# Kernel tuning notes

Hardware: AMD Instinct MI355X
Metric: run time of the kernel (lower is better)

## Reference

```python
import jax, jax.numpy as jnp
import numpy as np
import math

D = 512
H = 8
DH = D // H
B, T = 4, 2048


def _poly(x, coeffs):
    # iterative-power polynomial eval, same products as the Vandermonde matmul
    acc = coeffs[0] * jnp.ones_like(x)
    p = jnp.ones_like(x)
    for i in range(1, coeffs.shape[0]):
        p = p * x
        acc = acc + coeffs[i] * p
    return acc


def _exp_fn(x, exp_c):
    return jnp.maximum(_poly(x, exp_c), 1e-8)


def _softmax(x, exp_c):
    x = x - jnp.max(x, axis=-1, keepdims=True)
    e = _exp_fn(x, exp_c)
    return e / jnp.sum(e, axis=-1, keepdims=True)


def _gelu(x, gelu_c):
    return _poly(jnp.clip(x, -4.0, 4.0), gelu_c)


def _layernorm(x, gamma, beta):
    mean = jnp.mean(x, axis=-1, keepdims=True)
    var = jnp.mean(x * x, axis=-1, keepdims=True) - mean * mean
    v = var + 1e-5
    y = jnp.full_like(v, 0.5)
    for _ in range(3):  # Newton iterations for rsqrt
        y = y * (3.0 - v * y * y) * 0.5
    return (x - mean) * y * gamma + beta


def setup_inputs() -> dict:
    key = jax.random.key(0)
    ks = jax.random.split(key, 8)
    x = jax.random.normal(ks[0], (B, T, D), dtype=jnp.float32)
    s = 0.02
    Wq = jax.random.normal(ks[1], (D, D), dtype=jnp.float32) * s
    Wk = jax.random.normal(ks[2], (D, D), dtype=jnp.float32) * s
    Wv = jax.random.normal(ks[3], (D, D), dtype=jnp.float32) * s
    Wo = jax.random.normal(ks[4], (D, D), dtype=jnp.float32) * s
    W1 = jax.random.normal(ks[5], (D, 4 * D), dtype=jnp.float32) * s
    W2 = jax.random.normal(ks[6], (4 * D, D), dtype=jnp.float32) * s
    g1 = jnp.ones((D,), jnp.float32); b1 = jnp.zeros((D,), jnp.float32)
    g2 = jnp.ones((D,), jnp.float32); b2 = jnp.zeros((D,), jnp.float32)
    # GELU degree-7 least-squares fit on [-4,4]
    x_fit = jnp.linspace(-4.0, 4.0, 1000)
    y_fit = 0.5 * x_fit * (1.0 + jax.scipy.special.erf(x_fit / math.sqrt(2.0)))
    V = x_fit[:, None] ** jnp.arange(8)[None, :]
    gelu_c = jnp.linalg.lstsq(V, y_fit)[0].astype(jnp.float32)
    # exp Taylor coeffs degree 6
    exp_c = jnp.array([1.0 / math.factorial(i) for i in range(7)], dtype=jnp.float32)
    return dict(x=x, Wq=Wq, Wk=Wk, Wv=Wv, Wo=Wo, W1=W1, W2=W2,
                g1=g1, b1=b1, g2=g2, b2=b2, gelu_c=gelu_c, exp_c=exp_c)


def reference(x, Wq, Wk, Wv, Wo, W1, W2, g1, b1, g2, b2, gelu_c, exp_c):
    Bn, Tn, Dn = x.shape
    q = (x @ Wq).reshape(Bn, Tn, H, DH).transpose(0, 2, 1, 3)  # [B,H,T,dh]
    k = (x @ Wk).reshape(Bn, Tn, H, DH).transpose(0, 2, 1, 3)
    v = (x @ Wv).reshape(Bn, Tn, H, DH).transpose(0, 2, 1, 3)
    scores = jnp.einsum('bhqd,bhkd->bhqk', q, k) / math.sqrt(DH)
    attn = _softmax(scores, exp_c)
    out = jnp.einsum('bhqk,bhkd->bhqd', attn, v).transpose(0, 2, 1, 3).reshape(Bn, Tn, Dn)
    out = out @ Wo
    h = _layernorm(x + out, g1, b1)
    ffn = _gelu(h @ W1, gelu_c) @ W2
    return _layernorm(h + ffn, g2, b2)
```

## Files before the change

### kernel.cpp

```cpp
#include <hip/hip_runtime.h>
#include <hip/hip_bf16.h>

typedef __bf16 bf16_t;
typedef __bf16 bf16x8 __attribute__((ext_vector_type(8)));
typedef float f32x4 __attribute__((ext_vector_type(4)));

#define MFMA16(a, b, c) __builtin_amdgcn_mfma_f32_16x16x32_bf16((a), (b), (c), 0, 0, 0)

__device__ __forceinline__ void gl_lds16(const bf16_t* g, bf16_t* l) {
  __builtin_amdgcn_global_load_lds(
      (const __attribute__((address_space(1))) void*)g,
      (__attribute__((address_space(3))) void*)l, 16, 0, 0);
}

__device__ __forceinline__ unsigned pack_bf16(float a, float b) {
  union { bf16_t h[2]; unsigned u; } c;
  c.h[0] = (bf16_t)a; c.h[1] = (bf16_t)b;
  return c.u;
}

__global__ __launch_bounds__(256) void k_prep(
    const float* __restrict__ x, bf16_t* __restrict__ x_bf,
    const float* __restrict__ Wq, const float* __restrict__ Wk,
    const float* __restrict__ Wv, const float* __restrict__ Wo,
    const float* __restrict__ W1, const float* __restrict__ W2,
    bf16_t* __restrict__ WqkvT, bf16_t* __restrict__ WoT,
    bf16_t* __restrict__ W1T, bf16_t* __restrict__ W2T) {
  __shared__ float tile[64][65];
  int bid = blockIdx.x, tid = threadIdx.x;
  if (bid < 4096) {
    int i = bid * 256 + tid;
    float4 f = ((const float4*)x)[i];
    union { bf16_t h[4]; uint2 u; } cv;
    cv.h[0] = (bf16_t)f.x; cv.h[1] = (bf16_t)f.y;
    cv.h[2] = (bf16_t)f.z; cv.h[3] = (bf16_t)f.w;
    ((uint2*)x_bf)[i] = cv.u;
    return;
  }
  int t = bid - 4096;
  const float* W; bf16_t* WT; int K, N, idx, gx;
  if (t < 64)       { W = Wq; WT = WqkvT;                      K = 512;  N = 512;  idx = t;       gx = 8;  }
  else if (t < 128) { W = Wk; WT = WqkvT + (size_t)512 * 512;  K = 512;  N = 512;  idx = t - 64;  gx = 8;  }
  else if (t < 192) { W = Wv; WT = WqkvT + (size_t)1024 * 512; K = 512;  N = 512;  idx = t - 128; gx = 8;  }
  else if (t < 256) { W = Wo; WT = WoT;                        K = 512;  N = 512;  idx = t - 192; gx = 8;  }
  else if (t < 512) { W = W1; WT = W1T;                        K = 512;  N = 2048; idx = t - 256; gx = 8;  }
  else              { W = W2; WT = W2T;                        K = 2048; N = 512;  idx = t - 512; gx = 32; }
  int bk = (idx % gx) * 64, bn = (idx / gx) * 64;
  int tx = tid & 63, ty = tid >> 6;
  for (int i = ty; i < 64; i += 4)
    tile[i][tx] = W[(size_t)(bk + i) * N + bn + tx];
  __syncthreads();
  for (int i = ty; i < 64; i += 4)
    WT[(size_t)(bn + i) * K + bk + tx] = (bf16_t)tile[tx][i];
}

template <int MODE, int BM>
__global__ __launch_bounds__(256) void k_gemm_bt(
    const bf16_t* __restrict__ A, const bf16_t* __restrict__ Bt,
    float* __restrict__ Cf, bf16_t* __restrict__ Cb,
    bf16_t* __restrict__ Cb2, bf16_t* __restrict__ Cb3,
    int M, int N, int K, const float* __restrict__ coef) {
  __shared__ __align__(16) bf16_t As[2][BM * 32];
  __shared__ __align__(16) bf16_t Bs[2][128 * 32];
  constexpr int NF = (BM == 128) ? 4 : 2;
  int tid = threadIdx.x;
  int lane = tid & 63, wave = tid >> 6;
  int bm = blockIdx.x * BM, bn = blockIdx.y * 128;
  int wr = (BM == 128) ? (wave >> 1) * 64 : 0;
  int wc = (BM == 128) ? (wave & 1) * 64 : wave * 32;
  int lr = lane & 15, lk = (lane >> 4) * 8;
  int srow = tid >> 2, scol = (tid & 3) * 8;

  f32x4 zero = {0.f, 0.f, 0.f, 0.f};
  f32x4 acc[4][NF];
#pragma unroll
  for (int m = 0; m < 4; ++m)
#pragma unroll
    for (int n = 0; n < NF; ++n) acc[m][n] = zero;

  const bf16_t* pA = A + (size_t)(bm + srow) * K + scol;
  const bf16_t* pB = Bt + (size_t)(bn + srow) * K + scol;

  auto STAGE = [&](int buf, int k0) {
    bf16_t* lA = &As[buf][tid * 8];
    bf16_t* lB = &Bs[buf][tid * 8];
    gl_lds16(pA + k0, lA);
    if (BM == 128) gl_lds16(pA + (size_t)64 * K + k0, lA + 2048);
    gl_lds16(pB + k0, lB);
    gl_lds16(pB + (size_t)64 * K + k0, lB + 2048);
  };

  STAGE(0, 0);
  __syncthreads();
  int buf = 0;
  for (int k0 = 0; k0 < K; k0 += 32) {
    if (k0 + 32 < K) STAGE(buf ^ 1, k0 + 32);
    bf16x8 a[4], b[NF];
#pragma unroll
    for (int m = 0; m < 4; ++m) a[m] = *(const bf16x8*)&As[buf][(wr + m * 16 + lr) * 32 + lk];
#pragma unroll
    for (int n = 0; n < NF; ++n) b[n] = *(const bf16x8*)&Bs[buf][(wc + n * 16 + lr) * 32 + lk];
    __builtin_amdgcn_s_setprio(1);
#pragma unroll
    for (int m = 0; m < 4; ++m)
#pragma unroll
      for (int n = 0; n < NF; ++n)
        acc[m][n] = MFMA16(a[m], b[n], acc[m][n]);
    __builtin_amdgcn_s_setprio(0);
    __syncthreads();
    buf ^= 1;
  }

  float c8[8];
  if (MODE == 4) {
#pragma unroll
    for (int i = 0; i < 8; ++i) c8[i] = coef[i];
  }
  int rbase = (lane >> 4) * 4;
#pragma unroll
  for (int m = 0; m < 4; ++m) {
#pragma unroll
    for (int n = 0; n < NF; ++n) {
#pragma unroll
      for (int r = 0; r < 4; ++r) {
        int gm = bm + wr + m * 16 + rbase + r;
        int gn = bn + wc + n * 16 + lr;
        float v = acc[m][n][r];
        if (MODE == 0) {
          Cf[(size_t)gm * N + gn] = v;
        } else if (MODE == 4) {
          float xx = fminf(fmaxf(v, -4.f), 4.f);
          float p = c8[0], pw = 1.f;
#pragma unroll
          for (int i = 1; i < 8; ++i) { pw *= xx; p += c8[i] * pw; }
          Cb[(size_t)gm * N + gn] = (bf16_t)p;
        } else {
          int mat = gn >> 9, col = gn & 511;
          int b_ = gm >> 11, t_ = gm & 2047, h_ = col >> 6, d_ = col & 63;
          if (mat == 0) {
            Cb[(((size_t)b_ * 8 + h_) * 2048 + t_) * 64 + d_] = (bf16_t)(v * 0.125f);
          } else if (mat == 1) {
            int dsw = d_ ^ ((t_ & 7) << 3);
            Cb2[(((size_t)b_ * 8 + h_) * 2048 + t_) * 64 + dsw] = (bf16_t)v;
          } else {
            int tw = t_ & 63;
            int j = (((tw >> 2) & 3) << 1) | ((tw >> 4) & 1);
            int phys = (((tw & 32) << 1) + (j << 3) + ((tw & 3) << 1)) ^ ((d_ & 7) << 4);
            size_t e = ((((size_t)b_ * 8 + h_) * 64 + d_) * 4096 +
                        (size_t)(t_ >> 6) * 128 + phys) >> 1;
            Cb3[e] = (bf16_t)v;
          }
        }
      }
    }
  }
}

__global__ __launch_bounds__(256) void k_attn(
    const bf16_t* __restrict__ qb, const bf16_t* __restrict__ kb,
    const bf16_t* __restrict__ vtb, bf16_t* __restrict__ ob,
    const float* __restrict__ exp_c) {
  __shared__ __align__(16) bf16_t Ks[3][64 * 64];
  __shared__ __align__(16) bf16_t Vs[2][64 * 64];
  int tid = threadIdx.x, lane = tid & 63, wave = tid >> 6;
  int b0 = blockIdx.x;
  int bid = (b0 & 7) * 128 + (b0 >> 3);
  int qt = bid & 31, bh = bid >> 5;
  const size_t bho = (size_t)bh * (2048 * 64);
  const bf16_t* Q = qb + bho + (size_t)qt * 64 * 64;
  const bf16_t* Kp = kb + bho;
  const bf16_t* Vp = vtb + bho;
  int lr = lane & 15, lg = lane >> 4;

  bf16x8 qa[2];
#pragma unroll
  for (int h = 0; h < 2; ++h)
    qa[h] = *(const bf16x8*)&Q[(wave * 16 + lr) * 64 + h * 32 + lg * 8];

  float ec[7];
#pragma unroll
  for (int i = 0; i < 7; ++i) ec[i] = exp_c[i];

  union { unsigned u[4]; bf16x8 v; } ones;
#pragma unroll
  for (int i = 0; i < 4; ++i) ones.u[i] = 0x3f803f80u;

  int offA[4], offB[4];
#pragma unroll
  for (int n = 0; n < 4; ++n) {
    int row = n * 16 + lr, sw = (row & 7) << 4;
    offA[n] = (row * 128 + lg * 16) ^ sw;
    offB[n] = (row * 128 + 64 + lg * 16) ^ sw;
  }

  auto STAGE_K = [&](int buf, int kt) {
    bf16_t* lk = &Ks[buf][tid * 8];
    const bf16_t* gk = Kp + (size_t)kt * 4096 + tid * 8;
    gl_lds16(gk, lk);
    gl_lds16(gk + 2048, lk + 2048);
  };
  auto STAGE_V = [&](int buf, int kt) {
    bf16_t* lv = &Vs[buf][tid * 8];
    const bf16_t* gv = Vp + (size_t)(tid >> 3) * 2048 + kt * 64 + (tid & 7) * 8;
    gl_lds16(gv, lv);
    gl_lds16(gv + (size_t)32 * 2048, lv + 2048);
  };

  f32x4 zero = {0.f, 0.f, 0.f, 0.f};
  auto qk_tile = [&](const char* kbase, f32x4* sout) {
    __builtin_amdgcn_s_setprio(1);
#pragma unroll
    for (int n = 0; n < 4; ++n) {
      bf16x8 kb0 = *(const bf16x8*)(kbase + offA[n]);
      bf16x8 kb1 = *(const bf16x8*)(kbase + offB[n]);
      sout[n] = MFMA16(kb1, qa[1], MFMA16(kb0, qa[0], zero));
    }
    __builtin_amdgcn_s_setprio(0);
  };

  f32x4 oacc[4], oacc_s = zero;
#pragma unroll
  for (int n = 0; n < 4; ++n) oacc[n] = zero;

  f32x4 sA[4], sB[4];

  STAGE_K(0, 0);
  STAGE_K(1, 1);
  STAGE_V(0, 0);
  __syncthreads();
  qk_tile((const char*)Ks[0], sA);

  auto STEP = [&](int kt, f32x4* scur, f32x4* snext) {
    if (kt < 30) STAGE_K((kt + 2) % 3, kt + 2);
    if (kt < 31) STAGE_V((kt + 1) & 1, kt + 1);
    if (kt < 31) qk_tile((const char*)Ks[(kt + 1) % 3], snext);
    unsigned pk[4][2];
#pragma unroll
    for (int n = 0; n < 4; ++n) {
      float pf[4];
#pragma unroll
      for (int r = 0; r < 4; ++r) {
        float xv = scur[n][r];
        float p = ec[6];
#pragma unroll
        for (int i = 5; i >= 0; --i) p = __builtin_fmaf(p, xv, ec[i]);
        pf[r] = p;
      }
      pk[n][0] = pack_bf16(pf[0], pf[1]);
      pk[n][1] = pack_bf16(pf[2], pf[3]);
    }
    union { unsigned u[4]; bf16x8 v; } pa0, pa1;
    pa0.u[0] = pk[0][0]; pa0.u[1] = pk[0][1]; pa0.u[2] = pk[1][0]; pa0.u[3] = pk[1][1];
    pa1.u[0] = pk[2][0]; pa1.u[1] = pk[2][1]; pa1.u[2] = pk[3][0]; pa1.u[3] = pk[3][1];
    const char* vbase = (const char*)Vs[kt & 1];
    __builtin_amdgcn_s_setprio(1);
#pragma unroll
    for (int dd = 0; dd < 4; ++dd) {
      bf16x8 v0 = *(const bf16x8*)(vbase + offA[dd]);
      bf16x8 v1 = *(const bf16x8*)(vbase + offB[dd]);
      oacc[dd] = MFMA16(pa1.v, v1, MFMA16(pa0.v, v0, oacc[dd]));
    }
    oacc_s = MFMA16(pa1.v, ones.v, MFMA16(pa0.v, ones.v, oacc_s));
    __builtin_amdgcn_s_setprio(0);
    __syncthreads();
  };

  for (int it = 0; it < 16; ++it) {
    STEP(2 * it, sA, sB);
    STEP(2 * it + 1, sB, sA);
  }

  int b_ = bh >> 3, h_ = bh & 7;
#pragma unroll
  for (int dd = 0; dd < 4; ++dd)
#pragma unroll
    for (int r = 0; r < 4; ++r) {
      int t_ = qt * 64 + wave * 16 + lg * 4 + r;
      int d_ = dd * 16 + lr;
      float val = oacc[dd][r] / oacc_s[r];
      ob[(((size_t)b_ * 2048 + t_) * 8 + h_) * 64 + d_] = (bf16_t)val;
    }
}

__global__ __launch_bounds__(256) void k_ln(
    const float* __restrict__ xa, const float* __restrict__ xb,
    const float* __restrict__ gamma, const float* __restrict__ beta,
    float* __restrict__ outf, bf16_t* __restrict__ outb) {
  int row = blockIdx.x * 4 + (threadIdx.x >> 6);
  int lane = threadIdx.x & 63;
  const float* pa = xa + (size_t)row * 512;
  const float* pb = xb + (size_t)row * 512;
  float4 a0 = ((const float4*)pa)[lane];
  float4 a1 = ((const float4*)pa)[lane + 64];
  float4 b0 = ((const float4*)pb)[lane];
  float4 b1 = ((const float4*)pb)[lane + 64];
  float x[8] = {a0.x + b0.x, a0.y + b0.y, a0.z + b0.z, a0.w + b0.w,
                a1.x + b1.x, a1.y + b1.y, a1.z + b1.z, a1.w + b1.w};
  float s = 0.f, sq = 0.f;
#pragma unroll
  for (int i = 0; i < 8; ++i) { s += x[i]; sq += x[i] * x[i]; }
#pragma unroll
  for (int off = 1; off < 64; off <<= 1) {
    s += __shfl_xor(s, off);
    sq += __shfl_xor(sq, off);
  }
  float mean = s * (1.f / 512.f);
  float var = sq * (1.f / 512.f) - mean * mean;
  float v = var + 1e-5f;
  float y = 0.5f;
#pragma unroll
  for (int it = 0; it < 3; ++it) y = y * (3.0f - v * y * y) * 0.5f;

  float4 g0 = ((const float4*)gamma)[lane];
  float4 g1 = ((const float4*)gamma)[lane + 64];
  float4 e0 = ((const float4*)beta)[lane];
  float4 e1 = ((const float4*)beta)[lane + 64];
  float o[8];
  o[0] = (x[0] - mean) * y * g0.x + e0.x;
  o[1] = (x[1] - mean) * y * g0.y + e0.y;
  o[2] = (x[2] - mean) * y * g0.z + e0.z;
  o[3] = (x[3] - mean) * y * g0.w + e0.w;
  o[4] = (x[4] - mean) * y * g1.x + e1.x;
  o[5] = (x[5] - mean) * y * g1.y + e1.y;
  o[6] = (x[6] - mean) * y * g1.z + e1.z;
  o[7] = (x[7] - mean) * y * g1.w + e1.w;
  float* po = outf + (size_t)row * 512;
  ((float4*)po)[lane]      = make_float4(o[0], o[1], o[2], o[3]);
  ((float4*)po)[lane + 64] = make_float4(o[4], o[5], o[6], o[7]);
  if (outb) {
    bf16_t* pq = outb + (size_t)row * 512;
    union { bf16_t h[4]; uint2 u; } c0, c1;
    c0.h[0] = (bf16_t)o[0]; c0.h[1] = (bf16_t)o[1]; c0.h[2] = (bf16_t)o[2]; c0.h[3] = (bf16_t)o[3];
    c1.h[0] = (bf16_t)o[4]; c1.h[1] = (bf16_t)o[5]; c1.h[2] = (bf16_t)o[6]; c1.h[3] = (bf16_t)o[7];
    ((uint2*)pq)[lane]      = c0.u;
    ((uint2*)pq)[lane + 64] = c1.u;
  }
}

extern "C" void kernel_launch(void* const* d_in, const int* in_sizes, int n_in,
                              void* d_out, int out_size, void* d_ws, size_t ws_size,
                              hipStream_t stream) {
  const float* x      = (const float*)d_in[0];
  const float* Wq     = (const float*)d_in[1];
  const float* Wk     = (const float*)d_in[2];
  const float* Wv     = (const float*)d_in[3];
  const float* Wo     = (const float*)d_in[4];
  const float* W1     = (const float*)d_in[5];
  const float* W2     = (const float*)d_in[6];
  const float* g1     = (const float*)d_in[7];
  const float* b1     = (const float*)d_in[8];
  const float* g2     = (const float*)d_in[9];
  const float* b2     = (const float*)d_in[10];
  const float* gelu_c = (const float*)d_in[11];
  const float* exp_c  = (const float*)d_in[12];

  const int M = 8192;
  const size_t actBF = (size_t)M * 512 * 2;
  char* p = (char*)d_ws;
  auto carve = [&](size_t bytes) {
    void* r = (void*)p;
    p += (bytes + 255) & ~(size_t)255;
    return r;
  };
  bf16_t* x_bf   = (bf16_t*)carve(actBF);
  bf16_t* q_bf   = (bf16_t*)carve(actBF);
  bf16_t* k_bf   = (bf16_t*)carve(actBF);
  bf16_t* vT_bf  = (bf16_t*)carve(actBF);
  bf16_t* o_bf   = (bf16_t*)carve(actBF);
  bf16_t* h_bf   = (bf16_t*)carve(actBF);
  bf16_t* WqkvT  = (bf16_t*)carve((size_t)1536 * 512 * 2);
  bf16_t* WoT    = (bf16_t*)carve(512 * 512 * 2);
  bf16_t* W1T    = (bf16_t*)carve(512 * 2048 * 2);
  bf16_t* W2T    = (bf16_t*)carve(512 * 2048 * 2);
  bf16_t* g_bf   = (bf16_t*)carve((size_t)M * 2048 * 2);
  float*  proj   = (float*)carve((size_t)M * 512 * 4);
  float*  h_f    = (float*)carve((size_t)M * 512 * 4);
  float*  f2     = proj;

  k_prep<<<4864, 256, 0, stream>>>(x, x_bf, Wq, Wk, Wv, Wo, W1, W2,
                                   WqkvT, WoT, W1T, W2T);

  k_gemm_bt<5, 128><<<dim3(64, 12), 256, 0, stream>>>(
      x_bf, WqkvT, nullptr, q_bf, k_bf, vT_bf, M, 1536, 512, nullptr);

  k_attn<<<1024, 256, 0, stream>>>(q_bf, k_bf, vT_bf, o_bf, exp_c);

  k_gemm_bt<0, 64><<<dim3(128, 4), 256, 0, stream>>>(
      o_bf, WoT, proj, nullptr, nullptr, nullptr, M, 512, 512, nullptr);

  k_ln<<<2048, 256, 0, stream>>>(x, proj, g1, b1, h_f, h_bf);

  k_gemm_bt<4, 128><<<dim3(64, 16), 256, 0, stream>>>(
      h_bf, W1T, nullptr, g_bf, nullptr, nullptr, M, 2048, 512, gelu_c);

  k_gemm_bt<0, 64><<<dim3(128, 4), 256, 0, stream>>>(
      g_bf, W2T, f2, nullptr, nullptr, nullptr, M, 512, 2048, nullptr);

  k_ln<<<2048, 256, 0, stream>>>(h_f, f2, g2, b2, (float*)d_out, nullptr);
}
```

Before: 203.3 us.

## Process 128 query rows per attention block to reuse K/V tiles

The attention kernel now gives each wave two 16-row query sub-tiles, so a block covers 128 queries instead of 64 and the grid halves to 512 blocks. Each K and V tile staged into LDS is reused across twice as many queries, which halves global-to-LDS traffic and barrier count per query. In exchange it roughly doubles accumulator and score registers per thread, which may lower occupancy. With 512 blocks there are also fewer blocks to spread across the GPU's compute units.

```diff
diff --git a/kernel.cpp b/kernel.cpp
--- a/kernel.cpp
+++ b/kernel.cpp
@@ -164,18 +164,20 @@
   __shared__ __align__(16) bf16_t Vs[2][64 * 64];
   int tid = threadIdx.x, lane = tid & 63, wave = tid >> 6;
   int b0 = blockIdx.x;
-  int bid = (b0 & 7) * 128 + (b0 >> 3);
-  int qt = bid & 31, bh = bid >> 5;
+  int bid = (b0 & 7) * 64 + (b0 >> 3);
+  int qt = bid & 15, bh = bid >> 4;
   const size_t bho = (size_t)bh * (2048 * 64);
-  const bf16_t* Q = qb + bho + (size_t)qt * 64 * 64;
+  const bf16_t* Q = qb + bho + (size_t)qt * 128 * 64;
   const bf16_t* Kp = kb + bho;
   const bf16_t* Vp = vtb + bho;
   int lr = lane & 15, lg = lane >> 4;
 
-  bf16x8 qa[2];
-#pragma unroll
-  for (int h = 0; h < 2; ++h)
-    qa[h] = *(const bf16x8*)&Q[(wave * 16 + lr) * 64 + h * 32 + lg * 8];
+  bf16x8 qa[2][2];
+#pragma unroll
+  for (int j = 0; j < 2; ++j)
+#pragma unroll
+    for (int h = 0; h < 2; ++h)
+      qa[j][h] = *(const bf16x8*)&Q[(wave * 32 + j * 16 + lr) * 64 + h * 32 + lg * 8];
 
   float ec[7];
 #pragma unroll
@@ -207,22 +209,28 @@
   };
 
   f32x4 zero = {0.f, 0.f, 0.f, 0.f};
-  auto qk_tile = [&](const char* kbase, f32x4* sout) {
+  auto qk_tile = [&](const char* kbase, f32x4 (*sout)[4]) {
     __builtin_amdgcn_s_setprio(1);
 #pragma unroll
     for (int n = 0; n < 4; ++n) {
       bf16x8 kb0 = *(const bf16x8*)(kbase + offA[n]);
       bf16x8 kb1 = *(const bf16x8*)(kbase + offB[n]);
-      sout[n] = MFMA16(kb1, qa[1], MFMA16(kb0, qa[0], zero));
+#pragma unroll
+      for (int j = 0; j < 2; ++j)
+        sout[j][n] = MFMA16(kb1, qa[j][1], MFMA16(kb0, qa[j][0], zero));
     }
     __builtin_amdgcn_s_setprio(0);
   };
 
-  f32x4 oacc[4], oacc_s = zero;
-#pragma unroll
-  for (int n = 0; n < 4; ++n) oacc[n] = zero;
-
-  f32x4 sA[4], sB[4];
+  f32x4 oacc[2][4], oacc_s[2];
+#pragma unroll
+  for (int j = 0; j < 2; ++j) {
+#pragma unroll
+    for (int n = 0; n < 4; ++n) oacc[j][n] = zero;
+    oacc_s[j] = zero;
+  }
+
+  f32x4 sA[2][4], sB[2][4];
 
   STAGE_K(0, 0);
   STAGE_K(1, 1);
@@ -230,37 +238,46 @@
   __syncthreads();
   qk_tile((const char*)Ks[0], sA);
 
-  auto STEP = [&](int kt, f32x4* scur, f32x4* snext) {
+  auto STEP = [&](int kt, f32x4 (*scur)[4], f32x4 (*snext)[4]) {
     if (kt < 30) STAGE_K((kt + 2) % 3, kt + 2);
     if (kt < 31) STAGE_V((kt + 1) & 1, kt + 1);
     if (kt < 31) qk_tile((const char*)Ks[(kt + 1) % 3], snext);
-    unsigned pk[4][2];
-#pragma unroll
-    for (int n = 0; n < 4; ++n) {
-      float pf[4];
-#pragma unroll
-      for (int r = 0; r < 4; ++r) {
-        float xv = scur[n][r];
-        float p = ec[6];
-#pragma unroll
-        for (int i = 5; i >= 0; --i) p = __builtin_fmaf(p, xv, ec[i]);
-        pf[r] = p;
+    union { unsigned u[4]; bf16x8 v; } pa[2][2];
+#pragma unroll
+    for (int j = 0; j < 2; ++j) {
+      unsigned pk[4][2];
+#pragma unroll
+      for (int n = 0; n < 4; ++n) {
+        float pf[4];
+#pragma unroll
+        for (int r = 0; r < 4; ++r) {
+          float xv = scur[j][n][r];
+          float p = ec[6];
+#pragma unroll
+          for (int i = 5; i >= 0; --i) p = __builtin_fmaf(p, xv, ec[i]);
+          pf[r] = p;
+        }
+        pk[n][0] = pack_bf16(pf[0], pf[1]);
+        pk[n][1] = pack_bf16(pf[2], pf[3]);
       }
-      pk[n][0] = pack_bf16(pf[0], pf[1]);
-      pk[n][1] = pack_bf16(pf[2], pf[3]);
+      pa[j][0].u[0] = pk[0][0]; pa[j][0].u[1] = pk[0][1];
+      pa[j][0].u[2] = pk[1][0]; pa[j][0].u[3] = pk[1][1];
+      pa[j][1].u[0] = pk[2][0]; pa[j][1].u[1] = pk[2][1];
+      pa[j][1].u[2] = pk[3][0]; pa[j][1].u[3] = pk[3][1];
     }
-    union { unsigned u[4]; bf16x8 v; } pa0, pa1;
-    pa0.u[0] = pk[0][0]; pa0.u[1] = pk[0][1]; pa0.u[2] = pk[1][0]; pa0.u[3] = pk[1][1];
-    pa1.u[0] = pk[2][0]; pa1.u[1] = pk[2][1]; pa1.u[2] = pk[3][0]; pa1.u[3] = pk[3][1];
     const char* vbase = (const char*)Vs[kt & 1];
     __builtin_amdgcn_s_setprio(1);
 #pragma unroll
     for (int dd = 0; dd < 4; ++dd) {
       bf16x8 v0 = *(const bf16x8*)(vbase + offA[dd]);
       bf16x8 v1 = *(const bf16x8*)(vbase + offB[dd]);
-      oacc[dd] = MFMA16(pa1.v, v1, MFMA16(pa0.v, v0, oacc[dd]));
+#pragma unroll
+      for (int j = 0; j < 2; ++j)
+        oacc[j][dd] = MFMA16(pa[j][1].v, v1, MFMA16(pa[j][0].v, v0, oacc[j][dd]));
     }
-    oacc_s = MFMA16(pa1.v, ones.v, MFMA16(pa0.v, ones.v, oacc_s));
+#pragma unroll
+    for (int j = 0; j < 2; ++j)
+      oacc_s[j] = MFMA16(pa[j][1].v, ones.v, MFMA16(pa[j][0].v, ones.v, oacc_s[j]));
     __builtin_amdgcn_s_setprio(0);
     __syncthreads();
   };
@@ -272,14 +289,16 @@
 
   int b_ = bh >> 3, h_ = bh & 7;
 #pragma unroll
-  for (int dd = 0; dd < 4; ++dd)
-#pragma unroll
-    for (int r = 0; r < 4; ++r) {
-      int t_ = qt * 64 + wave * 16 + lg * 4 + r;
-      int d_ = dd * 16 + lr;
-      float val = oacc[dd][r] / oacc_s[r];
-      ob[(((size_t)b_ * 2048 + t_) * 8 + h_) * 64 + d_] = (bf16_t)val;
-    }
+  for (int j = 0; j < 2; ++j)
+#pragma unroll
+    for (int dd = 0; dd < 4; ++dd)
+#pragma unroll
+      for (int r = 0; r < 4; ++r) {
+        int t_ = qt * 128 + wave * 32 + j * 16 + lg * 4 + r;
+        int d_ = dd * 16 + lr;
+        float val = oacc[j][dd][r] / oacc_s[j][r];
+        ob[(((size_t)b_ * 2048 + t_) * 8 + h_) * 64 + d_] = (bf16_t)val;
+      }
 }
 
 __global__ __launch_bounds__(256) void k_ln(
@@ -383,7 +402,7 @@
   k_gemm_bt<5, 128><<<dim3(64, 12), 256, 0, stream>>>(
       x_bf, WqkvT, nullptr, q_bf, k_bf, vT_bf, M, 1536, 512, nullptr);
 
-  k_attn<<<1024, 256, 0, stream>>>(q_bf, k_bf, vT_bf, o_bf, exp_c);
+  k_attn<<<512, 256, 0, stream>>>(q_bf, k_bf, vT_bf, o_bf, exp_c);
 
   k_gemm_bt<0, 64><<<dim3(128, 4), 256, 0, stream>>>(
       o_bf, WoT, proj, nullptr, nullptr, nullptr, M, 512, 512, nullptr);
```

New measurement: 191.7 us. -5.7%, faster.
